# Kernel optimization log

Measured on AMD Instinct MI355X. Metric: run time of the kernel, lower is better.

Reference implementation:

```python
import jax, jax.numpy as jnp
import numpy as np
import math

B, S, D, H, L, FF, T = 2, 1024, 1024, 16, 8, 4096, 512
HD = D // H
EPS = 1e-5


def _ln(x, g, b):
    m = jnp.mean(x, axis=-1, keepdims=True)
    v = jnp.var(x, axis=-1, keepdims=True)
    return (x - m) * jax.lax.rsqrt(v + EPS) * g + b


def _rope(x, cos, sin):
    # x: [B,S,H,HD]; interleaved even/odd rotary as in _apply_rotary_emb_sincos
    xe, xo = x[..., 0::2], x[..., 1::2]
    c = cos[None, :, None, :]
    s = sin[None, :, None, :]
    return jnp.stack([xe * c - xo * s, xe * s + xo * c], axis=-1).reshape(x.shape)


def setup_inputs():
    key = jax.random.key(0)
    ks = iter(jax.random.split(key, 40))
    n = lambda shape, sc=0.02: jax.random.normal(next(ks), shape, jnp.float32) * sc
    return {
        "inputs_embeds": jax.random.normal(next(ks), (B, S, D), jnp.float32),
        "attention_mask": jnp.ones((B, 1, 1, S), jnp.float32),
        "time_step": jax.random.uniform(next(ks), (B,), jnp.float32),
        "wpe": n((S, D)),
        "ln1_g": jnp.ones((L, D)), "ln1_b": jnp.zeros((L, D)),
        "attn_w": n((L, D, 3 * D)), "attn_b": jnp.zeros((L, 3 * D)),
        "projw": n((L, D, D)), "projb": jnp.zeros((L, D)),
        "ln2_g": jnp.ones((L, D)), "ln2_b": jnp.zeros((L, D)),
        "fcw": n((L, D, FF)), "fcb": jnp.zeros((L, FF)),
        "pw2": n((L, FF, D)), "pb2": jnp.zeros((L, D)),
        "sst": n((L, 6, D), 1.0 / D ** 0.5),
        "te_w1": n((T, D)), "te_b1": jnp.zeros((D,)),
        "te_w2": n((D, D)), "te_b2": jnp.zeros((D,)),
        "ada_w": n((D, 6 * D)), "ada_b": jnp.zeros((6 * D,)),
        "lnf_g": jnp.ones((D,)), "lnf_b": jnp.zeros((D,)),
        "fsst": n((2, D), 1.0 / D ** 0.5),
        "out_w": n((D, D)), "out_b": jnp.zeros((D,)),
    }


def reference(inputs_embeds, attention_mask, time_step, wpe, ln1_g, ln1_b,
              attn_w, attn_b, projw, projb, ln2_g, ln2_b, fcw, fcb, pw2, pb2,
              sst, te_w1, te_b1, te_w2, te_b2, ada_w, ada_b, lnf_g, lnf_b,
              fsst, out_w, out_b):
    hs = inputs_embeds + wpe[:S][None]  # position embedding
    # rotary tables: [S, HD//2]
    half = HD // 2
    freqs = 1.0 / (10000.0 ** (jnp.arange(half, dtype=jnp.float32) * 2.0 / HD))
    ang = jnp.arange(S, dtype=jnp.float32)[:, None] * freqs[None]
    cos, sin = jnp.cos(ang), jnp.sin(ang)
    mask = (1.0 - attention_mask) * jnp.finfo(jnp.float32).min  # [B,1,1,S]
    # timestep embedding (flow_t_size=T, scale=1000, max_period=10000)
    halfT = T // 2
    tf = jnp.exp(-math.log(10000.0) * jnp.arange(halfT, dtype=jnp.float32) / halfT)
    targs = time_step[:, None] * tf[None] * 1000.0
    tproj = jnp.concatenate([jnp.cos(targs), jnp.sin(targs)], axis=-1)  # [B,T]
    emb = jax.nn.silu(tproj @ te_w1 + te_b1) @ te_w2 + te_b2  # [B,D]
    adaln = (jax.nn.silu(emb) @ ada_w + ada_b).reshape(B, 6, D)

    layer_params = dict(ln1_g=ln1_g, ln1_b=ln1_b, aw=attn_w, ab=attn_b,
                        pw=projw, pb=projb, ln2_g=ln2_g, ln2_b=ln2_b,
                        fw=fcw, fb=fcb, qw=pw2, qb=pb2, sst=sst)

    def block(h, p):
        mod = p["sst"][None] + adaln  # [B,6,D]
        sh1, sc1, g1, sh2, sc2, g2 = [mod[:, i:i + 1] for i in range(6)]
        res = h
        x = _ln(h, p["ln1_g"], p["ln1_b"]) * (1.0 + sc1) + sh1
        qkv = x @ p["aw"] + p["ab"]
        q, k, v = [t.reshape(B, S, H, HD) for t in jnp.split(qkv, 3, axis=-1)]
        q, k = _rope(q, cos, sin), _rope(k, cos, sin)
        scores = jnp.einsum("bqhd,bkhd->bhqk", q, k) / math.sqrt(HD) + mask
        attn = jax.nn.softmax(scores, axis=-1)
        o = jnp.einsum("bhqk,bkhd->bqhd", attn, v).reshape(B, S, D)
        o = o @ p["pw"] + p["pb"]
        h = o * g1 + res
        res = h
        x = _ln(h, p["ln2_g"], p["ln2_b"]) * (1.0 + sc2) + sh2
        x = jax.nn.gelu(x @ p["fw"] + p["fb"], approximate=True) @ p["qw"] + p["qb"]
        return x * g2 + res, None

    hs, _ = jax.lax.scan(block, hs, layer_params)
    fmod = fsst[None] + emb[:, None]  # [B,2,D]
    shift, scale = fmod[:, 0:1], fmod[:, 1:2]
    hs = _ln(hs, lnf_g, lnf_b) * (1.0 + scale) + shift
    return hs @ out_w + out_b
```

## Files before the change

### kernel.cpp

```cpp
#include <hip/hip_runtime.h>
#include <stdint.h>

typedef unsigned short u16;
typedef __attribute__((ext_vector_type(8))) short bf8_t;
typedef __attribute__((ext_vector_type(4))) float f4_t;

#define DEV static __device__ __forceinline__
#define MFMA16(a, b, c) __builtin_amdgcn_mfma_f32_16x16x32_bf16((a), (b), (c), 0, 0, 0)
#define GLDS(gp, lp) __builtin_amdgcn_global_load_lds((const __attribute__((address_space(1))) void*)(gp), \
                                                      (__attribute__((address_space(3))) void*)(lp), 16, 0, 0)

DEV u16 f2bf(float f) {
  union { float f; uint32_t u; } x; x.f = f;
  uint32_t r = x.u + 0x7FFFu + ((x.u >> 16) & 1u);
  return (u16)(r >> 16);
}

DEV void transpose_body(const float* __restrict__ W, u16* __restrict__ WT, int K, int N,
                        int n0, int k0, u16 (*tl)[66]) {
  const int t = threadIdx.x;
  const int tx = t & 15, ty = t >> 4;
  #pragma unroll
  for (int i = 0; i < 64; i += 16) {
    const float4 v = *(const float4*)&W[(long)(k0 + ty + i) * N + n0 + tx * 4];
    tl[tx * 4 + 0][ty + i] = f2bf(v.x);
    tl[tx * 4 + 1][ty + i] = f2bf(v.y);
    tl[tx * 4 + 2][ty + i] = f2bf(v.z);
    tl[tx * 4 + 3][ty + i] = f2bf(v.w);
  }
  __syncthreads();
  const int c = t & 15, r = t >> 4;
  #pragma unroll
  for (int i = 0; i < 64; i += 16) {
    const u16* p = &tl[r + i][c * 4];
    uint2 w;
    w.x = (uint32_t)p[0] | ((uint32_t)p[1] << 16);
    w.y = (uint32_t)p[2] | ((uint32_t)p[3] << 16);
    *(uint2*)&WT[(long)(n0 + r + i) * K + k0 + c * 4] = w;
  }
}

__global__ __launch_bounds__(256) void transpose_k(const float* __restrict__ W, u16* __restrict__ WT,
                                                   int K, int N) {
  __shared__ u16 tl[64][66];
  transpose_body(W, WT, K, N, blockIdx.x * 64, blockIdx.y * 64, tl);
}

__global__ __launch_bounds__(256)
void transpose4_k(const float* __restrict__ w0, u16* __restrict__ o0,
                  const float* __restrict__ w1, u16* __restrict__ o1,
                  const float* __restrict__ w2, u16* __restrict__ o2,
                  const float* __restrict__ w3, u16* __restrict__ o3) {
  __shared__ u16 tl[64][66];
  int bid = blockIdx.x;
  const float* W; u16* O; int K, N, nbx;
  if (bid < 768)        {             W = w0; O = o0; K = 1024; N = 3072; nbx = 48; }
  else if (bid < 1024)  { bid -= 768; W = w1; O = o1; K = 1024; N = 1024; nbx = 16; }
  else if (bid < 2048)  { bid -= 1024; W = w2; O = o2; K = 1024; N = 4096; nbx = 64; }
  else                  { bid -= 2048; W = w3; O = o3; K = 4096; N = 1024; nbx = 16; }
  transpose_body(W, O, K, N, (bid % nbx) * 64, (bid / nbx) * 64, tl);
}

enum { EPI_F32 = 0, EPI_GATE = 1, EPI_GELU = 2, EPI_RAW = 3 };

template <int BM, int EPI, int KS>
__global__ __launch_bounds__(256)
void gemm_bt(const u16* __restrict__ A, const u16* __restrict__ BT, const float* __restrict__ bias,
             float* outF, u16* outB, const float* gate, const float* res, int M, int N, int K) {
  constexpr int MI = BM / 32;
  __shared__ u16 sA[2][BM * 32];
  __shared__ u16 sB[2][128 * 32];
  const int tid = threadIdx.x, lane = tid & 63, wid = tid >> 6;
  const long rowBase = (long)blockIdx.x * BM;
  const long colBase = (long)blockIdx.y * 128;
  const int kz = (KS > 1) ? blockIdx.z : 0;
  const int kbeg = kz * (K / KS);
  const int wr = (wid >> 1) * (BM / 2), wc = (wid & 1) * 64;
  const int fr = lane & 15, kg = (lane >> 4) * 8;

  const f4_t zero = {0.0f, 0.0f, 0.0f, 0.0f};
  f4_t acc[MI][4];
  #pragma unroll
  for (int i = 0; i < MI; ++i)
    #pragma unroll
    for (int j = 0; j < 4; ++j) acc[i][j] = zero;

  const int sr = lane >> 2, scol = (lane & 3) * 8;
  const int c0 = wid * 2;
  const u16 *Ag0, *Ag1 = nullptr, *Bg0, *Bg1;
  int aoff0, aoff1 = 0, boff0, boff1;
  if constexpr (BM == 128) {
    Ag0 = A + (rowBase + c0 * 16 + sr) * (long)K + scol;
    Ag1 = A + (rowBase + c0 * 16 + 16 + sr) * (long)K + scol;
    aoff0 = (c0 * 16) * 32;
    aoff1 = (c0 * 16 + 16) * 32;
  } else {
    Ag0 = A + (rowBase + wid * 16 + sr) * (long)K + scol;
    aoff0 = (wid * 16) * 32;
  }
  Bg0 = BT + (colBase + c0 * 16 + sr) * (long)K + scol;
  Bg1 = BT + (colBase + c0 * 16 + 16 + sr) * (long)K + scol;
  boff0 = (c0 * 16) * 32;
  boff1 = (c0 * 16 + 16) * 32;

  auto stage = [&](int buf, int k0) {
    GLDS(Ag0 + k0, &sA[buf][aoff0]);
    if constexpr (BM == 128) GLDS(Ag1 + k0, &sA[buf][aoff1]);
    GLDS(Bg0 + k0, &sB[buf][boff0]);
    GLDS(Bg1 + k0, &sB[buf][boff1]);
  };

  const int nk = (K / KS) / 32;
  stage(0, kbeg);
  __syncthreads();
  int cur = 0;
  for (int t = 0; t < nk; ++t) {
    if (t + 1 < nk) stage(cur ^ 1, kbeg + (t + 1) * 32);
    bf8_t af[MI], bfv[4];
    #pragma unroll
    for (int m = 0; m < MI; ++m) af[m] = *(const bf8_t*)&sA[cur][(wr + m * 16 + fr) * 32 + kg];
    #pragma unroll
    for (int n = 0; n < 4; ++n) bfv[n] = *(const bf8_t*)&sB[cur][(wc + n * 16 + fr) * 32 + kg];
    #pragma unroll
    for (int m = 0; m < MI; ++m)
      #pragma unroll
      for (int n = 0; n < 4; ++n) acc[m][n] = MFMA16(af[m], bfv[n], acc[m][n]);
    __syncthreads();
    cur ^= 1;
  }

  const int r0 = (lane >> 4) * 4;
  #pragma unroll
  for (int m = 0; m < MI; ++m) {
    #pragma unroll
    for (int n = 0; n < 4; ++n) {
      const long col = colBase + wc + n * 16 + fr;
      const float bv = (EPI == EPI_RAW) ? 0.0f : bias[col];
      #pragma unroll
      for (int j = 0; j < 4; ++j) {
        const long row = rowBase + wr + m * 16 + r0 + j;
        float v = acc[m][n][j] + bv;
        if (EPI == EPI_F32) {
          outF[row * N + col] = v;
        } else if (EPI == EPI_RAW) {
          outF[((long)kz * M + row) * N + col] = v;
        } else if (EPI == EPI_GATE) {
          const int b = (int)(row >> 10);
          const float g = gate[(long)b * 6144 + col];
          outF[row * N + col] = v * g + res[row * N + col];
        } else {
          const float t = 0.7978845608028654f * (v + 0.044715f * v * v * v);
          const float e = __expf(2.0f * t);
          const float th = 1.0f - 2.0f / (e + 1.0f);
          outB[row * N + col] = f2bf(0.5f * v * (1.0f + th));
        }
      }
    }
  }
}

__global__ __launch_bounds__(256)
void ln_mod(const float* __restrict__ h, const float* __restrict__ gamma, const float* __restrict__ beta,
            const float* shp, const float* scp, int bstride, u16* __restrict__ xb) {
  const int row = blockIdx.x * 4 + (threadIdx.x >> 6);
  const int lane = threadIdx.x & 63;
  const int b = row >> 10;
  const long base = (long)row * 1024;
  f4_t x[4];
  float s = 0.0f;
  #pragma unroll
  for (int j = 0; j < 4; ++j) {
    x[j] = *(const f4_t*)&h[base + j * 256 + lane * 4];
    s += x[j][0] + x[j][1] + x[j][2] + x[j][3];
  }
  #pragma unroll
  for (int o = 32; o > 0; o >>= 1) s += __shfl_xor(s, o);
  const float mean = s * 0.0009765625f;
  float vs = 0.0f;
  #pragma unroll
  for (int j = 0; j < 4; ++j)
    #pragma unroll
    for (int e = 0; e < 4; ++e) { const float d = x[j][e] - mean; vs += d * d; }
  #pragma unroll
  for (int o = 32; o > 0; o >>= 1) vs += __shfl_xor(vs, o);
  const float inv = rsqrtf(vs * 0.0009765625f + 1e-5f);
  #pragma unroll
  for (int j = 0; j < 4; ++j) {
    const int col = j * 256 + lane * 4;
    const f4_t gg = *(const f4_t*)&gamma[col];
    const f4_t bb = *(const f4_t*)&beta[col];
    const f4_t sh = *(const f4_t*)&shp[(long)b * bstride + col];
    const f4_t sc = *(const f4_t*)&scp[(long)b * bstride + col];
    union { u16 u[4]; uint2 v; } pk;
    #pragma unroll
    for (int e = 0; e < 4; ++e)
      pk.u[e] = f2bf(((x[j][e] - mean) * inv * gg[e] + bb[e]) * (1.0f + sc[e]) + sh[e]);
    *(uint2*)&xb[base + col] = pk.v;
  }
}

__global__ __launch_bounds__(256)
void reduce_gate_ln(const float* __restrict__ part, const float* __restrict__ bias,
                    const float* __restrict__ gate, float* __restrict__ hs,
                    const float* __restrict__ gamma, const float* __restrict__ beta,
                    const float* shp, const float* scp, int bstride, u16* __restrict__ xb) {
  const int row = blockIdx.x * 4 + (threadIdx.x >> 6);
  const int lane = threadIdx.x & 63;
  const int b = row >> 10;
  const long base = (long)row * 1024;
  f4_t v[4];
  float s = 0.0f;
  #pragma unroll
  for (int j = 0; j < 4; ++j) {
    const int col = j * 256 + lane * 4;
    const f4_t p = *(const f4_t*)&part[base + col];
    const f4_t q = *(const f4_t*)&part[2048ll * 1024 + base + col];
    const f4_t bv = *(const f4_t*)&bias[col];
    const f4_t gv = *(const f4_t*)&gate[(long)b * 6144 + col];
    const f4_t r = *(const f4_t*)&hs[base + col];
    f4_t o;
    #pragma unroll
    for (int e = 0; e < 4; ++e) o[e] = (p[e] + q[e] + bv[e]) * gv[e] + r[e];
    *(f4_t*)&hs[base + col] = o;
    v[j] = o;
    s += o[0] + o[1] + o[2] + o[3];
  }
  #pragma unroll
  for (int o = 32; o > 0; o >>= 1) s += __shfl_xor(s, o);
  const float mean = s * 0.0009765625f;
  float vs = 0.0f;
  #pragma unroll
  for (int j = 0; j < 4; ++j)
    #pragma unroll
    for (int e = 0; e < 4; ++e) { const float d = v[j][e] - mean; vs += d * d; }
  #pragma unroll
  for (int o = 32; o > 0; o >>= 1) vs += __shfl_xor(vs, o);
  const float inv = rsqrtf(vs * 0.0009765625f + 1e-5f);
  #pragma unroll
  for (int j = 0; j < 4; ++j) {
    const int col = j * 256 + lane * 4;
    const f4_t gg = *(const f4_t*)&gamma[col];
    const f4_t bb = *(const f4_t*)&beta[col];
    const f4_t sh = *(const f4_t*)&shp[(long)b * bstride + col];
    const f4_t sc = *(const f4_t*)&scp[(long)b * bstride + col];
    union { u16 u[4]; uint2 v; } pk;
    #pragma unroll
    for (int e = 0; e < 4; ++e)
      pk.u[e] = f2bf(((v[j][e] - mean) * inv * gg[e] + bb[e]) * (1.0f + sc[e]) + sh[e]);
    *(uint2*)&xb[base + col] = pk.v;
  }
}

__global__ __launch_bounds__(256)
void rope_v(const float* __restrict__ qkv, const float* __restrict__ ct, const float* __restrict__ st,
            u16* __restrict__ qb, u16* __restrict__ kb, u16* __restrict__ vt) {
  __shared__ u16 tl[64][66];
  const int s0 = blockIdx.x * 64;
  const int h = blockIdx.y, b = blockIdx.z;
  const long bh = b * 16 + h;
  const int t = threadIdx.x;

  const int i = t & 31, r0 = t >> 5;
  #pragma unroll
  for (int which = 0; which < 2; ++which) {
    u16* op = which ? kb : qb;
    #pragma unroll
    for (int it = 0; it < 8; ++it) {
      const int s = s0 + r0 + it * 8;
      const float2 xx = *(const float2*)&qkv[(long)(b * 1024 + s) * 3072 + which * 1024 + h * 64 + 2 * i];
      const float c = ct[s * 32 + i], sn = st[s * 32 + i];
      const uint32_t w = (uint32_t)f2bf(xx.x * c - xx.y * sn) |
                         ((uint32_t)f2bf(xx.x * sn + xx.y * c) << 16);
      *(uint32_t*)&op[(bh * 1024 + s) * 64 + 2 * i] = w;
    }
  }

  const int tx = t & 15, ty = t >> 4;
  #pragma unroll
  for (int i2 = 0; i2 < 64; i2 += 16) {
    const float4 v = *(const float4*)&qkv[(long)(b * 1024 + s0 + ty + i2) * 3072 + 2048 + h * 64 + tx * 4];
    tl[tx * 4 + 0][ty + i2] = f2bf(v.x);
    tl[tx * 4 + 1][ty + i2] = f2bf(v.y);
    tl[tx * 4 + 2][ty + i2] = f2bf(v.z);
    tl[tx * 4 + 3][ty + i2] = f2bf(v.w);
  }
  __syncthreads();
  const int c2 = t & 15, r2 = t >> 4;
  #pragma unroll
  for (int i2 = 0; i2 < 64; i2 += 16) {
    const u16* p = &tl[r2 + i2][c2 * 4];
    uint2 w;
    w.x = (uint32_t)p[0] | ((uint32_t)p[1] << 16);
    w.y = (uint32_t)p[2] | ((uint32_t)p[3] << 16);
    *(uint2*)&vt[(bh * 64 + r2 + i2) * 1024 + s0 + c2 * 4] = w;
  }
}

DEV void attn_body(bf8_t (&kcur)[4][2], bf8_t (&knxt)[4][2], const bf8_t (&qf)[2],
                   f4_t (&oacc)[4], float& m, float& psum, int kc,
                   const u16* __restrict__ Kp, const u16* __restrict__ Vt,
                   const float* smadd, u16* myP, int fr, int g) {
  const f4_t zero = {0.0f, 0.0f, 0.0f, 0.0f};
  bf8_t vf[4][2];
  #pragma unroll
  for (int dt = 0; dt < 4; ++dt)
    #pragma unroll
    for (int ks = 0; ks < 2; ++ks)
      vf[dt][ks] = *(const bf8_t*)&Vt[(long)(dt * 16 + fr) * 1024 + kc + ks * 32 + g * 8];
  f4_t st[4];
  #pragma unroll
  for (int kt = 0; kt < 4; ++kt) {
    st[kt] = MFMA16(kcur[kt][0], qf[0], zero);
    st[kt] = MFMA16(kcur[kt][1], qf[1], st[kt]);
  }
  {
    const int kn = (kc + 64) & 1023;
    #pragma unroll
    for (int kt = 0; kt < 4; ++kt)
      #pragma unroll
      for (int dh = 0; dh < 2; ++dh)
        knxt[kt][dh] = *(const bf8_t*)&Kp[(long)(kn + kt * 16 + fr) * 64 + dh * 32 + g * 8];
  }
  float p[4][4];
  float cm = -3.402823466e38f;
  #pragma unroll
  for (int kt = 0; kt < 4; ++kt) {
    const f4_t ma = *(const f4_t*)&smadd[kc + kt * 16 + g * 4];
    #pragma unroll
    for (int j = 0; j < 4; ++j) {
      p[kt][j] = st[kt][j] * 0.125f + ma[j];
      cm = fmaxf(cm, p[kt][j]);
    }
  }
  cm = fmaxf(cm, __shfl_xor(cm, 16));
  cm = fmaxf(cm, __shfl_xor(cm, 32));
  const float nm = fmaxf(m, cm);
  const float sc = __expf(m - nm);
  m = nm;
  float ls = 0.0f;
  #pragma unroll
  for (int kt = 0; kt < 4; ++kt)
    #pragma unroll
    for (int j = 0; j < 4; ++j) {
      p[kt][j] = __expf(p[kt][j] - nm);
      ls += p[kt][j];
    }
  psum = psum * sc + ls;
  #pragma unroll
  for (int dt = 0; dt < 4; ++dt)
    #pragma unroll
    for (int j = 0; j < 4; ++j) oacc[dt][j] *= sc;
  #pragma unroll
  for (int kt = 0; kt < 4; ++kt) {
    const int kb = kt * 2 + (g >> 1);
    uint2 w;
    w.x = (uint32_t)f2bf(p[kt][0]) | ((uint32_t)f2bf(p[kt][1]) << 16);
    w.y = (uint32_t)f2bf(p[kt][2]) | ((uint32_t)f2bf(p[kt][3]) << 16);
    *(uint2*)&myP[(kb * 16 + fr) * 8 + (g & 1) * 4] = w;
  }
  bf8_t pa0 = *(const bf8_t*)&myP[(g * 16 + fr) * 8];
  bf8_t pa1 = *(const bf8_t*)&myP[((4 + g) * 16 + fr) * 8];
  #pragma unroll
  for (int dt = 0; dt < 4; ++dt) {
    oacc[dt] = MFMA16(vf[dt][0], pa0, oacc[dt]);
    oacc[dt] = MFMA16(vf[dt][1], pa1, oacc[dt]);
  }
}

__global__ __launch_bounds__(64)
void attn_k(const u16* __restrict__ qb, const u16* __restrict__ kb, const u16* __restrict__ vt,
            const float* __restrict__ amask, u16* __restrict__ ob) {
  __shared__ float smadd[1024];
  __shared__ u16 pl[1024];
  const int q0 = blockIdx.x * 16;
  const int h = blockIdx.y, b = blockIdx.z;
  const long bh = b * 16 + h;
  const int lane = threadIdx.x;
  const int fr = lane & 15, g = lane >> 4;

  #pragma unroll
  for (int i = 0; i < 4; ++i) {
    const int e = (lane + i * 64) * 4;
    const f4_t am = *(const f4_t*)&amask[b * 1024 + e];
    f4_t md;
    #pragma unroll
    for (int j = 0; j < 4; ++j) md[j] = (1.0f - am[j]) * -3.402823466e38f;
    *(f4_t*)&smadd[e] = md;
  }

  const u16* Q = qb + (bh * 1024 + q0) * 64;
  const u16* Kp = kb + bh * 1024 * 64;
  const u16* Vt = vt + bh * 64 * 1024;

  bf8_t qf[2];
  qf[0] = *(const bf8_t*)&Q[fr * 64 + g * 8];
  qf[1] = *(const bf8_t*)&Q[fr * 64 + 32 + g * 8];

  const f4_t zero = {0.0f, 0.0f, 0.0f, 0.0f};
  f4_t oacc[4];
  #pragma unroll
  for (int dt = 0; dt < 4; ++dt) oacc[dt] = zero;
  float m = -1e30f, psum = 0.0f;

  bf8_t kfA[4][2], kfB[4][2];
  #pragma unroll
  for (int kt = 0; kt < 4; ++kt)
    #pragma unroll
    for (int dh = 0; dh < 2; ++dh)
      kfA[kt][dh] = *(const bf8_t*)&Kp[(long)(kt * 16 + fr) * 64 + dh * 32 + g * 8];

  for (int kc = 0; kc < 1024; kc += 128) {
    attn_body(kfA, kfB, qf, oacc, m, psum, kc, Kp, Vt, smadd, pl, fr, g);
    attn_body(kfB, kfA, qf, oacc, m, psum, kc + 64, Kp, Vt, smadd, pl, fr, g);
  }

  float ts = psum + __shfl_xor(psum, 16);
  ts += __shfl_xor(ts, 32);
  const float inv = 1.0f / ts;
  const long qrow = (long)b * 1024 + q0 + fr;
  #pragma unroll
  for (int dt = 0; dt < 4; ++dt) {
    union { u16 u[4]; uint2 v; } pk;
    #pragma unroll
    for (int j = 0; j < 4; ++j) pk.u[j] = f2bf(oacc[dt][j] * inv);
    *(uint2*)&ob[qrow * 1024 + h * 64 + dt * 16 + g * 4] = pk.v;
  }
}

__global__ void rope_tables(float* ct, float* st) {
  const int i = blockIdx.x * 256 + threadIdx.x;
  const int s = i >> 5, k = i & 31;
  const float freq = __expf(-9.210340371976184f * (float)(2 * k) / 64.0f);
  const float a = (float)s * freq;
  ct[i] = cosf(a);
  st[i] = sinf(a);
}

__global__ void init_hs(const float* __restrict__ e, const float* __restrict__ wpe, float* __restrict__ hs) {
  const long i = (long)blockIdx.x * 256 + threadIdx.x;
  float4 a = ((const float4*)e)[i];
  const float4 w = ((const float4*)wpe)[i & 262143];
  a.x += w.x; a.y += w.y; a.z += w.z; a.w += w.w;
  ((float4*)hs)[i] = a;
}

__global__ __launch_bounds__(256)
void time_mlp1(const float* __restrict__ ts, const float* __restrict__ w1,
               const float* __restrict__ b1, float* __restrict__ h1) {
  __shared__ float red[8][32];
  const int dl = threadIdx.x & 31, sl = threadIdx.x >> 5;
  const int d = blockIdx.x * 32 + dl, b = blockIdx.y;
  const float tsv = ts[b];
  float acc = 0.0f;
  for (int j = sl * 64; j < sl * 64 + 64; ++j) {
    const float tf = __expf(-9.210340371976184f * (float)(j & 255) / 256.0f);
    const float a = tsv * tf * 1000.0f;
    const float val = (j < 256) ? cosf(a) : sinf(a);
    acc += val * w1[(long)j * 1024 + d];
  }
  red[sl][dl] = acc;
  __syncthreads();
  if (threadIdx.x < 32) {
    const int dd = blockIdx.x * 32 + threadIdx.x;
    float a = b1[dd];
    #pragma unroll
    for (int s = 0; s < 8; ++s) a += red[s][threadIdx.x];
    h1[b * 1024 + dd] = a / (1.0f + __expf(-a));
  }
}

__global__ __launch_bounds__(256)
void time_mlp2(const float* __restrict__ h1, const float* __restrict__ w2,
               const float* __restrict__ b2, float* __restrict__ emb) {
  __shared__ float red[8][32];
  const int dl = threadIdx.x & 31, sl = threadIdx.x >> 5;
  const int d = blockIdx.x * 32 + dl, b = blockIdx.y;
  float acc = 0.0f;
  for (int j = sl * 128; j < sl * 128 + 128; ++j) acc += h1[b * 1024 + j] * w2[(long)j * 1024 + d];
  red[sl][dl] = acc;
  __syncthreads();
  if (threadIdx.x < 32) {
    const int dd = blockIdx.x * 32 + threadIdx.x;
    float a = b2[dd];
    #pragma unroll
    for (int s = 0; s < 8; ++s) a += red[s][threadIdx.x];
    emb[b * 1024 + dd] = a;
  }
}

__global__ void adaln_part(const float* __restrict__ emb, const float* __restrict__ aw,
                           float* __restrict__ part) {
  const int j = blockIdx.x * 256 + threadIdx.x;
  const int b = blockIdx.y, kz = blockIdx.z;
  float acc = 0.0f;
  for (int k = kz * 128; k < kz * 128 + 128; ++k) {
    const float e = emb[b * 1024 + k];
    acc += (e / (1.0f + __expf(-e))) * aw[(long)k * 6144 + j];
  }
  part[((long)kz * 2 + b) * 6144 + j] = acc;
}

__global__ void adaln_reduce(const float* __restrict__ part, const float* __restrict__ ab,
                             float* __restrict__ adaln) {
  const int j = blockIdx.x * 256 + threadIdx.x;
  const int b = blockIdx.y;
  float acc = ab[j];
  #pragma unroll
  for (int kz = 0; kz < 8; ++kz) acc += part[((long)kz * 2 + b) * 6144 + j];
  adaln[b * 6144 + j] = acc;
}

__global__ void build_mods(const float* __restrict__ sst, const float* __restrict__ adaln,
                           const float* __restrict__ fsst, const float* __restrict__ emb,
                           float* __restrict__ modAll, float* __restrict__ fmod) {
  const int i = blockIdx.x * 256 + threadIdx.x;
  if (i < 98304) {
    const int d = i & 1023;
    const int rest = i >> 10;
    const int slot = rest % 6;
    const int t2 = rest / 6;
    const int bb = t2 & 1, l = t2 >> 1;
    modAll[i] = sst[(long)(l * 6 + slot) * 1024 + d] + adaln[bb * 6144 + slot * 1024 + d];
  } else if (i < 98304 + 4096) {
    const int j = i - 98304;
    const int d = j & 1023;
    const int slot = (j >> 10) & 1;
    const int bb = j >> 11;
    fmod[j] = fsst[slot * 1024 + d] + emb[bb * 1024 + d];
  }
}

extern "C" void kernel_launch(void* const* d_in, const int* in_sizes, int n_in,
                              void* d_out, int out_size, void* d_ws, size_t ws_size,
                              hipStream_t stream) {
  const float* inp_emb = (const float*)d_in[0];
  const float* amask  = (const float*)d_in[1];
  const float* tstep  = (const float*)d_in[2];
  const float* wpe    = (const float*)d_in[3];
  const float* ln1_g  = (const float*)d_in[4];
  const float* ln1_b  = (const float*)d_in[5];
  const float* attn_w = (const float*)d_in[6];
  const float* attn_b = (const float*)d_in[7];
  const float* projw  = (const float*)d_in[8];
  const float* projb  = (const float*)d_in[9];
  const float* ln2_g  = (const float*)d_in[10];
  const float* ln2_b  = (const float*)d_in[11];
  const float* fcw    = (const float*)d_in[12];
  const float* fcb    = (const float*)d_in[13];
  const float* pw2    = (const float*)d_in[14];
  const float* pb2    = (const float*)d_in[15];
  const float* sst    = (const float*)d_in[16];
  const float* te_w1  = (const float*)d_in[17];
  const float* te_b1  = (const float*)d_in[18];
  const float* te_w2  = (const float*)d_in[19];
  const float* te_b2  = (const float*)d_in[20];
  const float* ada_w  = (const float*)d_in[21];
  const float* ada_b  = (const float*)d_in[22];
  const float* lnf_g  = (const float*)d_in[23];
  const float* lnf_b  = (const float*)d_in[24];
  const float* fsst   = (const float*)d_in[25];
  const float* out_w  = (const float*)d_in[26];
  const float* out_b  = (const float*)d_in[27];
  float* out = (float*)d_out;
  (void)in_sizes; (void)n_in; (void)out_size; (void)ws_size;

  char* wsb = (char*)d_ws;
  size_t off = 0;
  auto alloc = [&](size_t bytes) -> void* {
    void* p = wsb + off;
    off += (bytes + 255) & ~(size_t)255;
    return p;
  };
  u16* wtA = (u16*)alloc(3072ll * 1024 * 2);
  u16* wtP = (u16*)alloc(1024ll * 1024 * 2);
  u16* wtF = (u16*)alloc(4096ll * 1024 * 2);
  u16* wtQ = (u16*)alloc(1024ll * 4096 * 2);
  u16* wtO = (u16*)alloc(1024ll * 1024 * 2);
  float* hs   = (float*)alloc(2048ll * 1024 * 4);
  float* qkv  = (float*)alloc(2048ll * 3072 * 4);
  u16*   ffb  = (u16*)qkv;
  float* part = (float*)alloc(2ll * 2048 * 1024 * 4);
  u16* xb = (u16*)alloc(2048ll * 1024 * 2);
  u16* qb = (u16*)alloc(2048ll * 1024 * 2);
  u16* kb = (u16*)alloc(2048ll * 1024 * 2);
  u16* vt = (u16*)alloc(2048ll * 1024 * 2);
  u16* ob = (u16*)alloc(2048ll * 1024 * 2);
  float* ct    = (float*)alloc(32768 * 4);
  float* st    = (float*)alloc(32768 * 4);
  float* h1    = (float*)alloc(2 * 1024 * 4);
  float* emb   = (float*)alloc(2 * 1024 * 4);
  float* adaln = (float*)alloc(2 * 6144 * 4);
  float* modAll = (float*)alloc(8ll * 2 * 6 * 1024 * 4);
  float* fmod   = (float*)alloc(2 * 2 * 1024 * 4);

  rope_tables<<<128, 256, 0, stream>>>(ct, st);
  init_hs<<<2048, 256, 0, stream>>>(inp_emb, wpe, hs);
  time_mlp1<<<dim3(32, 2), 256, 0, stream>>>(tstep, te_w1, te_b1, h1);
  time_mlp2<<<dim3(32, 2), 256, 0, stream>>>(h1, te_w2, te_b2, emb);
  adaln_part<<<dim3(24, 2, 8), 256, 0, stream>>>(emb, ada_w, part);
  adaln_reduce<<<dim3(24, 2), 256, 0, stream>>>(part, ada_b, adaln);
  build_mods<<<400, 256, 0, stream>>>(sst, adaln, fsst, emb, modAll, fmod);
  transpose_k<<<dim3(16, 16), 256, 0, stream>>>(out_w, wtO, 1024, 1024);

  ln_mod<<<512, 256, 0, stream>>>(hs, ln1_g, ln1_b, modAll + 0 * 1024, modAll + 1 * 1024, 6144, xb);

  for (int l = 0; l < 8; ++l) {
    const float* ml = modAll + (long)l * 12288;
    transpose4_k<<<3072, 256, 0, stream>>>(attn_w + (long)l * 1024 * 3072, wtA,
                                           projw + (long)l * 1024 * 1024, wtP,
                                           fcw + (long)l * 1024 * 4096, wtF,
                                           pw2 + (long)l * 4096 * 1024, wtQ);

    gemm_bt<128, EPI_F32, 1><<<dim3(16, 24), 256, 0, stream>>>(xb, wtA, attn_b + l * 3072,
                                                               qkv, nullptr, nullptr, nullptr, 2048, 3072, 1024);
    rope_v<<<dim3(16, 16, 2), 256, 0, stream>>>(qkv, ct, st, qb, kb, vt);
    attn_k<<<dim3(64, 16, 2), 64, 0, stream>>>(qb, kb, vt, amask, ob);
    gemm_bt<64, EPI_GATE, 1><<<dim3(32, 8), 256, 0, stream>>>(ob, wtP, projb + l * 1024,
                                                              hs, nullptr, ml + 2 * 1024, hs, 2048, 1024, 1024);
    ln_mod<<<512, 256, 0, stream>>>(hs, ln2_g + l * 1024, ln2_b + l * 1024,
                                    ml + 3 * 1024, ml + 4 * 1024, 6144, xb);
    gemm_bt<128, EPI_GELU, 1><<<dim3(16, 32), 256, 0, stream>>>(xb, wtF, fcb + l * 4096,
                                                                nullptr, ffb, nullptr, nullptr, 2048, 4096, 1024);
    gemm_bt<128, EPI_RAW, 2><<<dim3(16, 8, 2), 256, 0, stream>>>(ffb, wtQ, nullptr,
                                                                 part, nullptr, nullptr, nullptr, 2048, 1024, 4096);
    if (l < 7) {
      const float* mln = modAll + (long)(l + 1) * 12288;
      reduce_gate_ln<<<512, 256, 0, stream>>>(part, pb2 + l * 1024, ml + 5 * 1024, hs,
                                              ln1_g + (l + 1) * 1024, ln1_b + (l + 1) * 1024,
                                              mln + 0 * 1024, mln + 1 * 1024, 6144, xb);
    } else {
      reduce_gate_ln<<<512, 256, 0, stream>>>(part, pb2 + l * 1024, ml + 5 * 1024, hs,
                                              lnf_g, lnf_b, fmod + 0, fmod + 1024, 2048, xb);
    }
  }

  gemm_bt<64, EPI_F32, 1><<<dim3(32, 8), 256, 0, stream>>>(xb, wtO, out_b,
                                                           out, nullptr, nullptr, nullptr, 2048, 1024, 1024);
}
```

Baseline: 1.855 ms.

## Split-K QKV GEMM with bias folded into rope, lazy softmax rescale, remap attention blocks

The QKV projection now uses a split-K of 2 that writes raw partials. The rope/V-transpose kernel sums the two partials and adds the bias, which gives the GEMM more blocks to spread across CUs. In attention, the running max and the accumulator rescale are updated only when the new block max exceeds the current max by more than 8 in some lane, which skips exp and multiply work. The attention grid is flattened with a head-interleaved block ordering, likely to spread work across XCDs or caches. The costs are an extra partial buffer in global memory, a second read per element in rope, and a larger intermediate that grows workspace use.

After: 1.875 ms. Within noise of the previous version (+1.1%).

```diff
diff --git a/kernel.cpp b/kernel.cpp
--- a/kernel.cpp
+++ b/kernel.cpp
@@ -252,37 +252,46 @@
 }
 
 __global__ __launch_bounds__(256)
-void rope_v(const float* __restrict__ qkv, const float* __restrict__ ct, const float* __restrict__ st,
+void rope_v(const float* __restrict__ qp, const float* __restrict__ bias,
+            const float* __restrict__ ct, const float* __restrict__ st,
             u16* __restrict__ qb, u16* __restrict__ kb, u16* __restrict__ vt) {
   __shared__ u16 tl[64][66];
   const int s0 = blockIdx.x * 64;
   const int h = blockIdx.y, b = blockIdx.z;
   const long bh = b * 16 + h;
   const int t = threadIdx.x;
+  const long PSTRIDE = 2048ll * 3072;
 
   const int i = t & 31, r0 = t >> 5;
   #pragma unroll
   for (int which = 0; which < 2; ++which) {
     u16* op = which ? kb : qb;
+    const float2 bv = *(const float2*)&bias[which * 1024 + h * 64 + 2 * i];
     #pragma unroll
     for (int it = 0; it < 8; ++it) {
       const int s = s0 + r0 + it * 8;
-      const float2 xx = *(const float2*)&qkv[(long)(b * 1024 + s) * 3072 + which * 1024 + h * 64 + 2 * i];
+      const long roff = (long)(b * 1024 + s) * 3072 + which * 1024 + h * 64 + 2 * i;
+      const float2 x0 = *(const float2*)&qp[roff];
+      const float2 x1 = *(const float2*)&qp[PSTRIDE + roff];
+      const float xe = x0.x + x1.x + bv.x, xo = x0.y + x1.y + bv.y;
       const float c = ct[s * 32 + i], sn = st[s * 32 + i];
-      const uint32_t w = (uint32_t)f2bf(xx.x * c - xx.y * sn) |
-                         ((uint32_t)f2bf(xx.x * sn + xx.y * c) << 16);
+      const uint32_t w = (uint32_t)f2bf(xe * c - xo * sn) |
+                         ((uint32_t)f2bf(xe * sn + xo * c) << 16);
       *(uint32_t*)&op[(bh * 1024 + s) * 64 + 2 * i] = w;
     }
   }
 
   const int tx = t & 15, ty = t >> 4;
+  const f4_t bv4 = *(const f4_t*)&bias[2048 + h * 64 + tx * 4];
   #pragma unroll
   for (int i2 = 0; i2 < 64; i2 += 16) {
-    const float4 v = *(const float4*)&qkv[(long)(b * 1024 + s0 + ty + i2) * 3072 + 2048 + h * 64 + tx * 4];
-    tl[tx * 4 + 0][ty + i2] = f2bf(v.x);
-    tl[tx * 4 + 1][ty + i2] = f2bf(v.y);
-    tl[tx * 4 + 2][ty + i2] = f2bf(v.z);
-    tl[tx * 4 + 3][ty + i2] = f2bf(v.w);
+    const long roff = (long)(b * 1024 + s0 + ty + i2) * 3072 + 2048 + h * 64 + tx * 4;
+    const f4_t v0 = *(const f4_t*)&qp[roff];
+    const f4_t v1 = *(const f4_t*)&qp[PSTRIDE + roff];
+    tl[tx * 4 + 0][ty + i2] = f2bf(v0[0] + v1[0] + bv4[0]);
+    tl[tx * 4 + 1][ty + i2] = f2bf(v0[1] + v1[1] + bv4[1]);
+    tl[tx * 4 + 2][ty + i2] = f2bf(v0[2] + v1[2] + bv4[2]);
+    tl[tx * 4 + 3][ty + i2] = f2bf(v0[3] + v1[3] + bv4[3]);
   }
   __syncthreads();
   const int c2 = t & 15, r2 = t >> 4;
@@ -334,22 +343,25 @@
   }
   cm = fmaxf(cm, __shfl_xor(cm, 16));
   cm = fmaxf(cm, __shfl_xor(cm, 32));
-  const float nm = fmaxf(m, cm);
-  const float sc = __expf(m - nm);
-  m = nm;
+  if (!__all(cm - m <= 8.0f)) {
+    const float nm = fmaxf(m, cm);
+    const float sc = __expf(m - nm);
+    psum *= sc;
+    #pragma unroll
+    for (int dt = 0; dt < 4; ++dt)
+      #pragma unroll
+      for (int j = 0; j < 4; ++j) oacc[dt][j] *= sc;
+    m = nm;
+  }
   float ls = 0.0f;
   #pragma unroll
   for (int kt = 0; kt < 4; ++kt)
     #pragma unroll
     for (int j = 0; j < 4; ++j) {
-      p[kt][j] = __expf(p[kt][j] - nm);
+      p[kt][j] = __expf(p[kt][j] - m);
       ls += p[kt][j];
     }
-  psum = psum * sc + ls;
-  #pragma unroll
-  for (int dt = 0; dt < 4; ++dt)
-    #pragma unroll
-    for (int j = 0; j < 4; ++j) oacc[dt][j] *= sc;
+  psum += ls;
   #pragma unroll
   for (int kt = 0; kt < 4; ++kt) {
     const int kb = kt * 2 + (g >> 1);
@@ -372,8 +384,14 @@
             const float* __restrict__ amask, u16* __restrict__ ob) {
   __shared__ float smadd[1024];
   __shared__ u16 pl[1024];
-  const int q0 = blockIdx.x * 16;
-  const int h = blockIdx.y, b = blockIdx.z;
+  const int bid = blockIdx.x;
+  const int c = bid & 7;
+  const int rest = bid >> 3;
+  const int qi = rest & 63;
+  const int tt = rest >> 6;
+  const int h = c + ((tt & 1) << 3);
+  const int b = tt >> 1;
+  const int q0 = qi * 16;
   const long bh = b * 16 + h;
   const int lane = threadIdx.x;
   const int fr = lane & 15, g = lane >> 4;
@@ -577,9 +595,8 @@
   u16* wtQ = (u16*)alloc(1024ll * 4096 * 2);
   u16* wtO = (u16*)alloc(1024ll * 1024 * 2);
   float* hs   = (float*)alloc(2048ll * 1024 * 4);
-  float* qkv  = (float*)alloc(2048ll * 3072 * 4);
-  u16*   ffb  = (u16*)qkv;
-  float* part = (float*)alloc(2ll * 2048 * 1024 * 4);
+  u16* ffb    = (u16*)alloc(2048ll * 4096 * 2);
+  float* part = (float*)alloc(2ll * 2048 * 3072 * 4);
   u16* xb = (u16*)alloc(2048ll * 1024 * 2);
   u16* qb = (u16*)alloc(2048ll * 1024 * 2);
   u16* kb = (u16*)alloc(2048ll * 1024 * 2);
@@ -611,10 +628,10 @@
                                            fcw + (long)l * 1024 * 4096, wtF,
                                            pw2 + (long)l * 4096 * 1024, wtQ);
 
-    gemm_bt<128, EPI_F32, 1><<<dim3(16, 24), 256, 0, stream>>>(xb, wtA, attn_b + l * 3072,
-                                                               qkv, nullptr, nullptr, nullptr, 2048, 3072, 1024);
-    rope_v<<<dim3(16, 16, 2), 256, 0, stream>>>(qkv, ct, st, qb, kb, vt);
-    attn_k<<<dim3(64, 16, 2), 64, 0, stream>>>(qb, kb, vt, amask, ob);
+    gemm_bt<128, EPI_RAW, 2><<<dim3(16, 24, 2), 256, 0, stream>>>(xb, wtA, nullptr,
+                                                                  part, nullptr, nullptr, nullptr, 2048, 3072, 1024);
+    rope_v<<<dim3(16, 16, 2), 256, 0, stream>>>(part, attn_b + l * 3072, ct, st, qb, kb, vt);
+    attn_k<<<2048, 64, 0, stream>>>(qb, kb, vt, amask, ob);
     gemm_bt<64, EPI_GATE, 1><<<dim3(32, 8), 256, 0, stream>>>(ob, wtP, projb + l * 1024,
                                                               hs, nullptr, ml + 2 * 1024, hs, 2048, 1024, 1024);
     ln_mod<<<512, 256, 0, stream>>>(hs, ln2_g + l * 1024, ln2_b + l * 1024,
```
